# Kernel tuning notes

Measured on AMD Instinct MI355X. Metric: run time of the kernel, lower is better.

## Reference

```python
import jax, jax.numpy as jnp
import numpy as np

ALPHA = 1.0
BETA = 0.05


def setup_inputs() -> dict:
    key = jax.random.key(0)
    kQ, kK, kV, kH, kDQ, kDK = jax.random.split(key, 6)
    N, M, D, d = 8192, 8192, 128, 128
    Q = jax.random.normal(kQ, (N, D), dtype=jnp.float32)
    K = jax.random.normal(kK, (M, D), dtype=jnp.float32)
    V = jax.random.normal(kV, (M, d), dtype=jnp.float32)
    # Doob h-potential must be strictly positive (it is logged)
    h = jax.random.uniform(kH, (N,), dtype=jnp.float32, minval=0.5, maxval=1.5)
    log_d_q = 0.1 * jax.random.normal(kDQ, (N,), dtype=jnp.float32)
    log_d_k = 0.1 * jax.random.normal(kDK, (M,), dtype=jnp.float32)
    return {"Q": Q, "K": K, "V": V, "h": h, "log_d_q": log_d_q, "log_d_k": log_d_k}


def reference(Q, K, V, h, log_d_q, log_d_k):
    # s_ij = -beta*||q_i - k_j||^2 - alpha*(log_d_q[i] + log_d_k[j]) + log h_i - log h_j
    q_norm2 = jnp.sum(Q * Q, axis=-1)  # (N,)
    k_norm2 = jnp.sum(K * K, axis=-1)  # (M,)
    log_h = jnp.log(h)                  # (N,) ; Q and K share h (self-attention points)
    qk = jnp.einsum("nd,md->nm", Q, K)  # (N, M)
    s = BETA * (2.0 * qk - q_norm2[:, None] - k_norm2[None, :])
    s = s - ALPHA * (log_d_q[:, None] + log_d_k[None, :])
    s = s + log_h[:, None] - log_h[None, :]
    # row-softmax = Markov normalisation; lse = log row sums of un-normalised kernel
    lse = jax.nn.logsumexp(s, axis=-1)          # (N,)
    P = jnp.exp(s - lse[:, None])               # (N, M)
    out = jnp.einsum("nm,md->nd", P, V)          # (N, d)
    return out, lse
```

## Files before the change

### kernel.cpp

```cpp
#include <hip/hip_runtime.h>
#include <cstddef>
#include <cstdint>

#define BETA 0.05f

typedef unsigned short u16;
typedef unsigned int u32;
typedef __attribute__((ext_vector_type(8))) short bf16x8;
typedef __attribute__((ext_vector_type(16))) float f32x16;
typedef __attribute__((ext_vector_type(4))) u32 u32x4;

constexpr int NQ = 8192;
constexpr int NK = 8192;
constexpr int DH = 128;
constexpr int SPLITS = 8;
constexpr int CHUNK = NK / SPLITS;
constexpr int KVB = 64;
constexpr int STEPS = CHUNK / KVB;


__device__ __forceinline__ u16 f2bf(float x) {
  union { float f; u32 u; } v; v.f = x;
  u32 r = (v.u + 0x7fffu + ((v.u >> 16) & 1u)) >> 16;
  return (u16)r;
}
__device__ __forceinline__ float fexp2(float x) {
#if __has_builtin(__builtin_amdgcn_exp2f)
  return __builtin_amdgcn_exp2f(x);
#else
  return exp2f(x);
#endif
}

__global__ void prep_qk(const float* __restrict__ Q, const float* __restrict__ ldq,
                        const float* __restrict__ K, const float* __restrict__ ldk,
                        const float* __restrict__ h, u16* __restrict__ Qa,
                        u16* __restrict__ Kf, float* __restrict__ B2f,
                        float* __restrict__ arow) {
  const int bi = blockIdx.x;
  const int lane = threadIdx.x & 63;
  if (bi < NQ / 4) {
    const int row = bi * 4 + (threadIdx.x >> 6);
    const float2 q2 = *(const float2*)(Q + (size_t)row * DH + lane * 2);
    float sq = q2.x * q2.x + q2.y * q2.y;
#pragma unroll
    for (int off = 32; off > 0; off >>= 1) sq += __shfl_xor(sq, off);
    const float SC = 2.0f * BETA * 1.4426950408889634f;
    ushort2 o; o.x = f2bf(SC * q2.x); o.y = f2bf(SC * q2.y);
    *(ushort2*)(Qa + (size_t)row * DH + lane * 2) = o;
    if (lane == 0) arow[row] = -BETA * sq - ldq[row] + logf(h[row]);
  } else {
    const int row = (bi - NQ / 4) * 4 + (threadIdx.x >> 6);
    const float2 k2 = *(const float2*)(K + (size_t)row * DH + lane * 2);
    float sq = k2.x * k2.x + k2.y * k2.y;
#pragma unroll
    for (int off = 32; off > 0; off >>= 1) sq += __shfl_xor(sq, off);
    ushort2 o; o.x = f2bf(k2.x); o.y = f2bf(k2.y);
    char* dst = (char*)Kf + ((size_t)(row >> 5) * 8 + (lane >> 3)) * 1024
              + ((((lane >> 2) & 1) * 32) + (row & 31)) * 16 + (lane & 3) * 4;
    *(ushort2*)dst = o;
    if (lane == 0) {
      const float b2 = (-BETA * sq - ldk[row] - logf(h[row])) * 1.4426950408889634f;
      const int w = row & 31;
      B2f[(size_t)(row >> 5) * 32 + ((w >> 2) & 1) * 16 + (w & 3) + 4 * (w >> 3)] = b2;
    }
  }
}

__global__ void prep_vt(const float* __restrict__ V, u16* __restrict__ Vf) {
  __shared__ float tile[64][65];
  const int j0 = blockIdx.x * 64;
  const int d0 = blockIdx.y * 64;
  const int t = threadIdx.x;
  const int r = t >> 4;
  const int c = (t & 15) * 4;
#pragma unroll
  for (int rr = r; rr < 64; rr += 16) {
    const float4 v = *(const float4*)(V + (size_t)(j0 + rr) * DH + d0 + c);
    tile[rr][c + 0] = v.x; tile[rr][c + 1] = v.y;
    tile[rr][c + 2] = v.z; tile[rr][c + 3] = v.w;
  }
  __syncthreads();
  const int kv8i = t & 7;
  const int dl0 = t >> 3;
#pragma unroll
  for (int dd = dl0; dd < 64; dd += 32) {
    const int dg = d0 + dd;
    const int b16g = (j0 >> 4) + (kv8i >> 1);
    const int hi = kv8i & 1;
    union { u32x4 q; u16 s[8]; } pk;
#pragma unroll
    for (int m = 0; m < 8; ++m) pk.s[m] = f2bf(tile[kv8i * 8 + m][dd]);
    *(u32x4*)((char*)Vf + ((size_t)(b16g * 4 + (dg >> 5)) * 1024)
              + ((hi * 32) + (dg & 31)) * 16) = pk.q;
  }
}

__device__ __forceinline__ void smpv(const f32x16& s, const bf16x8 v[8],
                                     f32x16 acc[4], float& lsum, int hi) {
  float p[16];
#pragma unroll
  for (int r = 0; r < 16; ++r) p[r] = fexp2(s[r]);
  {
    float t0 = (p[0] + p[1]) + (p[2] + p[3]);
    float t1 = (p[4] + p[5]) + (p[6] + p[7]);
    float t2 = (p[8] + p[9]) + (p[10] + p[11]);
    float t3 = (p[12] + p[13]) + (p[14] + p[15]);
    lsum += (t0 + t1) + (t2 + t3);
  }
  u32 pk0, pk1, pk2, pk3, pk4, pk5, pk6, pk7;
  asm("v_cvt_pk_bf16_f32 %0, %1, %2" : "=v"(pk0) : "v"(p[0]),  "v"(p[1]));
  asm("v_cvt_pk_bf16_f32 %0, %1, %2" : "=v"(pk1) : "v"(p[2]),  "v"(p[3]));
  asm("v_cvt_pk_bf16_f32 %0, %1, %2" : "=v"(pk2) : "v"(p[4]),  "v"(p[5]));
  asm("v_cvt_pk_bf16_f32 %0, %1, %2" : "=v"(pk3) : "v"(p[6]),  "v"(p[7]));
  asm("v_cvt_pk_bf16_f32 %0, %1, %2" : "=v"(pk4) : "v"(p[8]),  "v"(p[9]));
  asm("v_cvt_pk_bf16_f32 %0, %1, %2" : "=v"(pk5) : "v"(p[10]), "v"(p[11]));
  asm("v_cvt_pk_bf16_f32 %0, %1, %2" : "=v"(pk6) : "v"(p[12]), "v"(p[13]));
  asm("v_cvt_pk_bf16_f32 %0, %1, %2" : "=v"(pk7) : "v"(p[14]), "v"(p[15]));
  const bool hb = (hi != 0);
#pragma unroll
  for (int ksl = 0; ksl < 2; ++ksl) {
    const u32 a0 = ksl ? pk4 : pk0, a1 = ksl ? pk5 : pk1;
    const u32 b0 = ksl ? pk6 : pk2, b1 = ksl ? pk7 : pk3;
    const u32 own0 = hb ? b0 : a0, own1 = hb ? b1 : a1;
    const u32 snd0 = hb ? a0 : b0, snd1 = hb ? a1 : b1;
    const u32 rcv0 = (u32)__shfl_xor((int)snd0, 32);
    const u32 rcv1 = (u32)__shfl_xor((int)snd1, 32);
    union { u32x4 u; bf16x8 b; } pa;
    pa.u[0] = hb ? rcv0 : own0;
    pa.u[1] = hb ? rcv1 : own1;
    pa.u[2] = hb ? own0 : rcv0;
    pa.u[3] = hb ? own1 : rcv1;
    __builtin_amdgcn_s_setprio(1);
#pragma unroll
    for (int dt = 0; dt < 4; ++dt)
      acc[dt] = __builtin_amdgcn_mfma_f32_32x32x16_bf16(pa.b, v[ksl * 4 + dt], acc[dt], 0, 0, 0);
    __builtin_amdgcn_s_setprio(0);
  }
}

__global__ __launch_bounds__(512, 2) void attn_main(
    const u16* __restrict__ Qa, const u16* __restrict__ Kf,
    const u16* __restrict__ Vf, const float* __restrict__ B2f,
    u16* __restrict__ Opart, float* __restrict__ Lpart) {
  const int tid = threadIdx.x;
  const int wid = tid >> 6;
  const int lane = tid & 63;
  const int hi = lane >> 5;
  const int ln31 = lane & 31;
  const int bi = blockIdx.x;
  const int ks = bi & 7;
  const int qg = bi >> 3;
  const int kvbase = ks * CHUNK;
  const int qrow0 = qg * 256 + wid * 32;

  bf16x8 qf[8];
#pragma unroll
  for (int sl = 0; sl < 8; ++sl)
    qf[sl] = *(const bf16x8*)((const char*)Qa + (size_t)(qrow0 + ln31) * 256 + sl * 32 + hi * 16);

  f32x16 acc[4];
#pragma unroll
  for (int dt = 0; dt < 4; ++dt)
#pragma unroll
    for (int r = 0; r < 16; ++r) acc[dt][r] = 0.0f;
  float lsum = 0.0f;

  const char* kfb = (const char*)Kf + ((size_t)(kvbase >> 5) * 8) * 1024 + lane * 16;
  const char* vfb = (const char*)Vf + ((size_t)(kvbase >> 4) * 4) * 1024 + lane * 16;
  const char* b2b = (const char*)B2f + (size_t)(kvbase >> 5) * 128 + hi * 64;

  bf16x8 k0[8], k1[8], v0[8], v1[8];
#pragma unroll
  for (int sl = 0; sl < 8; ++sl) k0[sl] = *(const bf16x8*)(kfb + sl * 1024);

  for (int t = 0; t < STEPS; ++t) {
    const char* kstep = kfb + (size_t)t * 16384;
    const char* vstep = vfb + (size_t)t * 16384;
    const char* b2step = b2b + (size_t)t * 256;

    f32x16 s0 = *(const f32x16*)(b2step);
    f32x16 s1 = *(const f32x16*)(b2step + 128);

#pragma unroll
    for (int i = 0; i < 8; ++i) v0[i] = *(const bf16x8*)(vstep + i * 1024);

    __builtin_amdgcn_s_setprio(1);
#pragma unroll
    for (int sl = 0; sl < 8; ++sl)
      s0 = __builtin_amdgcn_mfma_f32_32x32x16_bf16(k0[sl], qf[sl], s0, 0, 0, 0);
    __builtin_amdgcn_s_setprio(0);

#pragma unroll
    for (int sl = 0; sl < 8; ++sl) k1[sl] = *(const bf16x8*)(kstep + 8192 + sl * 1024);

    smpv(s0, v0, acc, lsum, hi);

    if (t + 1 < STEPS) {
#pragma unroll
      for (int sl = 0; sl < 8; ++sl) k0[sl] = *(const bf16x8*)(kstep + 16384 + sl * 1024);
    }
#pragma unroll
    for (int i = 0; i < 8; ++i) v1[i] = *(const bf16x8*)(vstep + 8192 + i * 1024);

    __builtin_amdgcn_s_setprio(1);
#pragma unroll
    for (int sl = 0; sl < 8; ++sl)
      s1 = __builtin_amdgcn_mfma_f32_32x32x16_bf16(k1[sl], qf[sl], s1, 0, 0, 0);
    __builtin_amdgcn_s_setprio(0);

    smpv(s1, v1, acc, lsum, hi);
  }

  lsum += __shfl_xor(lsum, 32);
  u16* op = Opart + ((size_t)ks * NQ + qrow0) * DH;
#pragma unroll
  for (int dt = 0; dt < 4; ++dt)
#pragma unroll
    for (int r = 0; r < 16; ++r) {
      const int q = (r & 3) + 8 * (r >> 2) + 4 * hi;
      op[(size_t)q * DH + dt * 32 + ln31] = f2bf(acc[dt][r]);
    }
  if (hi == 0) Lpart[(size_t)ks * NQ + qrow0 + ln31] = lsum;
}

__global__ void combine(const u16* __restrict__ Opart, const float* __restrict__ Lpart,
                        const float* __restrict__ arow, float* __restrict__ out,
                        float* __restrict__ lse) {
  const int idx = blockIdx.x * 256 + threadIdx.x;
  const int row = idx >> 5;
  const int d4 = (idx & 31) * 4;
  float o0 = 0.f, o1 = 0.f, o2 = 0.f, o3 = 0.f;
  float L = 0.f;
#pragma unroll
  for (int s = 0; s < SPLITS; ++s) {
    const ushort4 v = *(const ushort4*)(Opart + ((size_t)s * NQ + row) * DH + d4);
    union { u32 u; float f; } c0, c1, c2, c3;
    c0.u = ((u32)v.x) << 16; c1.u = ((u32)v.y) << 16;
    c2.u = ((u32)v.z) << 16; c3.u = ((u32)v.w) << 16;
    o0 += c0.f; o1 += c1.f; o2 += c2.f; o3 += c3.f;
    L += Lpart[(size_t)s * NQ + row];
  }
  const float inv = 1.0f / L;
  *(float4*)(out + (size_t)row * DH + d4) =
      make_float4(o0 * inv, o1 * inv, o2 * inv, o3 * inv);
  if ((idx & 31) == 0) lse[row] = logf(L) + arow[row];
}

extern "C" void kernel_launch(void* const* d_in, const int* in_sizes, int n_in,
                              void* d_out, int out_size, void* d_ws, size_t ws_size,
                              hipStream_t stream) {
  const float* Q = (const float*)d_in[0];
  const float* K = (const float*)d_in[1];
  const float* V = (const float*)d_in[2];
  const float* h = (const float*)d_in[3];
  const float* ldq = (const float*)d_in[4];
  const float* ldk = (const float*)d_in[5];

  char* ws = (char*)d_ws;
  u16* Qa    = (u16*)(ws + 0);
  u16* Kf    = (u16*)(ws + 2097152);
  u16* Vf    = (u16*)(ws + 4194304);
  float* B2f   = (float*)(ws + 6291456);
  float* arow  = (float*)(ws + 6324224);
  u16* Opart = (u16*)(ws + 6356992);
  float* Lpart = (float*)(ws + 23134208);

  float* out = (float*)d_out;
  float* lse = out + (size_t)NQ * DH;

  prep_qk<<<NQ / 2, 256, 0, stream>>>(Q, ldq, K, ldk, h, Qa, Kf, B2f, arow);
  prep_vt<<<dim3(NK / 64, DH / 64), 256, 0, stream>>>(V, Vf);
  attn_main<<<(NQ / 256) * SPLITS, 512, 0, stream>>>(Qa, Kf, Vf, B2f, Opart, Lpart);
  combine<<<NQ * 32 / 256, 256, 0, stream>>>(Opart, Lpart, arow, out, lse);
}
```

Measured before the change: 67.08 us.

## Stage K/V tiles through LDS with double-buffered global_load_lds

In the old kernel each of the 8 waves loaded the same K/V tiles from global memory straight into registers. The new kernel has the whole block cooperatively copy each K/V step into a double-buffered LDS region using direct global-to-LDS loads. The B2 bias row is also preloaded once into LDS. Waves then read operands from LDS, with a block barrier at the end of each step. This cuts redundant global/L2 traffic by about 8x, at the cost of about 68KB of LDS, a per-step __syncthreads, and dropping the occupancy hint of 2 blocks per CU.

New measurement: 57.21 us. -14.7%, faster.

```diff
diff --git a/kernel.cpp b/kernel.cpp
--- a/kernel.cpp
+++ b/kernel.cpp
@@ -17,6 +17,9 @@
 constexpr int CHUNK = NK / SPLITS;
 constexpr int KVB = 64;
 constexpr int STEPS = CHUNK / KVB;
+constexpr int KSTEP = 16384;
+constexpr int VSTEP = 16384;
+constexpr int LDS_BYTES = 2 * KSTEP + 2 * VSTEP + 4096;
 
 
 __device__ __forceinline__ u16 f2bf(float x) {
@@ -30,6 +33,11 @@
 #else
   return exp2f(x);
 #endif
+}
+__device__ __forceinline__ void gload_lds16(const void* gsrc, void* ldst) {
+  __builtin_amdgcn_global_load_lds(
+      (const __attribute__((address_space(1))) u32*)gsrc,
+      (__attribute__((address_space(3))) u32*)ldst, 16, 0, 0);
 }
 
 __global__ void prep_qk(const float* __restrict__ Q, const float* __restrict__ ldq,
@@ -139,10 +147,15 @@
   }
 }
 
-__global__ __launch_bounds__(512, 2) void attn_main(
+__global__ __launch_bounds__(512) void attn_main(
     const u16* __restrict__ Qa, const u16* __restrict__ Kf,
     const u16* __restrict__ Vf, const float* __restrict__ B2f,
     u16* __restrict__ Opart, float* __restrict__ Lpart) {
+  extern __shared__ __align__(16) char lds[];
+  char* ldsK = lds;
+  char* ldsV = lds + 2 * KSTEP;
+  char* ldsB = lds + 2 * KSTEP + 2 * VSTEP;
+
   const int tid = threadIdx.x;
   const int wid = tid >> 6;
   const int lane = tid & 63;
@@ -166,50 +179,60 @@
     for (int r = 0; r < 16; ++r) acc[dt][r] = 0.0f;
   float lsum = 0.0f;
 
-  const char* kfb = (const char*)Kf + ((size_t)(kvbase >> 5) * 8) * 1024 + lane * 16;
-  const char* vfb = (const char*)Vf + ((size_t)(kvbase >> 4) * 4) * 1024 + lane * 16;
-  const char* b2b = (const char*)B2f + (size_t)(kvbase >> 5) * 128 + hi * 64;
-
-  bf16x8 k0[8], k1[8], v0[8], v1[8];
-#pragma unroll
-  for (int sl = 0; sl < 8; ++sl) k0[sl] = *(const bf16x8*)(kfb + sl * 1024);
+  const char* KfG = (const char*)Kf + ((size_t)(kvbase >> 5) * 8) * 1024 + lane * 16;
+  const char* VfG = (const char*)Vf + ((size_t)(kvbase >> 4) * 4) * 1024 + lane * 16;
+
+  auto STAGE = [&](int buf, int step) {
+    const char* ksrc = KfG + (size_t)step * KSTEP + wid * 2048;
+    const char* vsrc = VfG + (size_t)step * VSTEP + wid * 2048;
+    char* kdst = ldsK + buf * KSTEP + wid * 2048;
+    char* vdst = ldsV + buf * VSTEP + wid * 2048;
+    gload_lds16(ksrc, kdst);
+    gload_lds16(ksrc + 1024, kdst + 1024);
+    gload_lds16(vsrc, vdst);
+    gload_lds16(vsrc + 1024, vdst + 1024);
+  };
+
+  if (wid < 4)
+    gload_lds16((const char*)B2f + (size_t)(kvbase >> 5) * 128 + wid * 1024 + lane * 16,
+                ldsB + wid * 1024);
+  STAGE(0, 0);
+  __syncthreads();
 
   for (int t = 0; t < STEPS; ++t) {
-    const char* kstep = kfb + (size_t)t * 16384;
-    const char* vstep = vfb + (size_t)t * 16384;
-    const char* b2step = b2b + (size_t)t * 256;
-
-    f32x16 s0 = *(const f32x16*)(b2step);
-    f32x16 s1 = *(const f32x16*)(b2step + 128);
-
-#pragma unroll
-    for (int i = 0; i < 8; ++i) v0[i] = *(const bf16x8*)(vstep + i * 1024);
-
+    const int cur = t & 1;
+    if (t < STEPS - 1) STAGE(cur ^ 1, t + 1);
+
+    const char* kb = ldsK + cur * KSTEP + lane * 16;
+    const char* vb = ldsV + cur * VSTEP + lane * 16;
+
+    f32x16 s0 = *(const f32x16*)(ldsB + t * 256 + hi * 64);
+    f32x16 s1 = *(const f32x16*)(ldsB + t * 256 + 128 + hi * 64);
+
+    bf16x8 kv[8], vv[8];
+#pragma unroll
+    for (int sl = 0; sl < 8; ++sl) kv[sl] = *(const bf16x8*)(kb + sl * 1024);
     __builtin_amdgcn_s_setprio(1);
 #pragma unroll
     for (int sl = 0; sl < 8; ++sl)
-      s0 = __builtin_amdgcn_mfma_f32_32x32x16_bf16(k0[sl], qf[sl], s0, 0, 0, 0);
+      s0 = __builtin_amdgcn_mfma_f32_32x32x16_bf16(kv[sl], qf[sl], s0, 0, 0, 0);
     __builtin_amdgcn_s_setprio(0);
-
-#pragma unroll
-    for (int sl = 0; sl < 8; ++sl) k1[sl] = *(const bf16x8*)(kstep + 8192 + sl * 1024);
-
-    smpv(s0, v0, acc, lsum, hi);
-
-    if (t + 1 < STEPS) {
-#pragma unroll
-      for (int sl = 0; sl < 8; ++sl) k0[sl] = *(const bf16x8*)(kstep + 16384 + sl * 1024);
-    }
-#pragma unroll
-    for (int i = 0; i < 8; ++i) v1[i] = *(const bf16x8*)(vstep + 8192 + i * 1024);
-
+#pragma unroll
+    for (int i = 0; i < 8; ++i) vv[i] = *(const bf16x8*)(vb + i * 1024);
+    smpv(s0, vv, acc, lsum, hi);
+
+#pragma unroll
+    for (int sl = 0; sl < 8; ++sl) kv[sl] = *(const bf16x8*)(kb + (8 + sl) * 1024);
     __builtin_amdgcn_s_setprio(1);
 #pragma unroll
     for (int sl = 0; sl < 8; ++sl)
-      s1 = __builtin_amdgcn_mfma_f32_32x32x16_bf16(k1[sl], qf[sl], s1, 0, 0, 0);
+      s1 = __builtin_amdgcn_mfma_f32_32x32x16_bf16(kv[sl], qf[sl], s1, 0, 0, 0);
     __builtin_amdgcn_s_setprio(0);
-
-    smpv(s1, v1, acc, lsum, hi);
+#pragma unroll
+    for (int i = 0; i < 8; ++i) vv[i] = *(const bf16x8*)(vb + (8 + i) * 1024);
+    smpv(s1, vv, acc, lsum, hi);
+
+    __syncthreads();
   }
 
   lsum += __shfl_xor(lsum, 32);
@@ -269,8 +292,11 @@
   float* out = (float*)d_out;
   float* lse = out + (size_t)NQ * DH;
 
+  hipFuncSetAttribute(reinterpret_cast<const void*>(attn_main),
+                      hipFuncAttributeMaxDynamicSharedMemorySize, LDS_BYTES);
+
   prep_qk<<<NQ / 2, 256, 0, stream>>>(Q, ldq, K, ldk, h, Qa, Kf, B2f, arow);
   prep_vt<<<dim3(NK / 64, DH / 64), 256, 0, stream>>>(V, Vf);
-  attn_main<<<(NQ / 256) * SPLITS, 512, 0, stream>>>(Qa, Kf, Vf, B2f, Opart, Lpart);
+  attn_main<<<(NQ / 256) * SPLITS, 512, LDS_BYTES, stream>>>(Qa, Kf, Vf, B2f, Opart, Lpart);
   combine<<<NQ * 32 / 256, 256, 0, stream>>>(Opart, Lpart, arow, out, lse);
 }
```
